# Optimization experiments

Measured on AMD Instinct MI355X. Metric: run time of the kernel, lower is better.

The kernel has to match this reference:

```python
import jax, jax.numpy as jnp
import numpy as np

B, N, K = 4, 4096, 16
D_POINTS, D_MODEL = 64, 128


def setup_inputs() -> dict:
    key = jax.random.key(0)
    ks = jax.random.split(key, 18)
    rn = lambda k, shp, s=0.05: (jax.random.normal(k, shp, jnp.float32) * s)
    return {
        "xyz": jax.random.normal(ks[0], (B, N, 3), jnp.float32),
        "features": jax.random.normal(ks[1], (B, N, D_POINTS), jnp.float32),
        # fc_delta: Linear(3,d_model) -> ReLU -> Linear(d_model,d_model)
        "Wd1": rn(ks[2], (3, D_MODEL)), "bd1": rn(ks[3], (D_MODEL,)),
        "Wd2": rn(ks[4], (D_MODEL, D_MODEL)), "bd2": rn(ks[5], (D_MODEL,)),
        # fc1: Linear(d_points, d_model)
        "Wf1": rn(ks[6], (D_POINTS, D_MODEL)), "bf1": rn(ks[7], (D_MODEL,)),
        # w_qs / w_ks / w_vs: Linear(d_model, d_model, bias=False)
        "Wq": rn(ks[8], (D_MODEL, D_MODEL)),
        "Wk": rn(ks[9], (D_MODEL, D_MODEL)),
        "Wv": rn(ks[10], (D_MODEL, D_MODEL)),
        # fc_gamma: Linear(d_model,d_model) -> ReLU -> Linear(d_model,d_model)
        "Wg1": rn(ks[11], (D_MODEL, D_MODEL)), "bg1": rn(ks[12], (D_MODEL,)),
        "Wg2": rn(ks[13], (D_MODEL, D_MODEL)), "bg2": rn(ks[14], (D_MODEL,)),
        # fc2: Linear(d_model, d_points)
        "Wo": rn(ks[15], (D_MODEL, D_POINTS)), "bo": rn(ks[16], (D_POINTS,)),
    }


def reference(xyz, features, Wd1, bd1, Wd2, bd2, Wf1, bf1, Wq, Wk, Wv,
              Wg1, bg1, Wg2, bg2, Wo, bo):
    sq = jnp.sum(xyz * xyz, axis=-1)
    d2 = sq[:, :, None] + sq[:, None, :] - 2.0 * jnp.einsum('bnd,bmd->bnm', xyz, xyz)
    # argsort()[:, :, :k] == k smallest distances (self included)
    _, knn_idx = jax.lax.top_k(-d2, K)  # [B,N,K] int32

    gather = jax.vmap(lambda a, i: a[i])  # per-batch fancy gather along point axis
    knn_xyz = gather(xyz, knn_idx)                       # [B,N,K,3]
    rel = xyz[:, :, None, :] - knn_xyz                   # [B,N,K,3]
    pos_enc = jax.nn.relu(rel @ Wd1 + bd1) @ Wd2 + bd2   # [B,N,K,D]

    shortcut = features
    f = features @ Wf1 + bf1                             # [B,N,D]
    knn_f = gather(f, knn_idx)                           # [B,N,K,D]

    q = f @ Wq                                           # [B,N,D]
    k = knn_f @ Wk                                       # [B,N,K,D]
    v = knn_f @ Wv                                       # [B,N,K,D]

    attn = q[:, :, None, :] - k + pos_enc                # [B,N,K,D]
    attn = jax.nn.relu(attn @ Wg1 + bg1) @ Wg2 + bg2
    attn = jax.nn.softmax(attn / np.sqrt(D_MODEL).astype(np.float32), axis=-2)

    res = jnp.einsum('bnkf,bnkf->bnf', attn, v + pos_enc)  # [B,N,D]
    return res @ Wo + bo + shortcut                        # [B,N,d_points]
```

## Files before the change

kernel.cpp:

```cpp
#include <hip/hip_runtime.h>
#include <hip/hip_bf16.h>

#define NPTS 4096
#define BATCH 4
#define BN (BATCH * NPTS)
#define DMODEL 128
#define DPTS 64
#define KNBR 16
#define SWS 136
#define PBLK 8

typedef unsigned short u16;
typedef unsigned int u32;
typedef unsigned long long u64;
typedef short bh8 __attribute__((ext_vector_type(8)));
typedef float f32x4 __attribute__((ext_vector_type(4)));

__device__ __forceinline__ float bfu(u16 u) {
    union { u32 i; float f; } c; c.i = ((u32)u) << 16; return c.f;
}
__device__ __forceinline__ u16 f2u(float x) {
    u32 u = __float_as_uint(x);
    u32 r = u + 0x7FFFu + ((u >> 16) & 1u);
    return (u16)(r >> 16);
}
__device__ __forceinline__ u32 pack2(float a, float b) {
    return (u32)f2u(a) | ((u32)f2u(b) << 16);
}
__device__ __forceinline__ u32 dpp_xor1(u32 v) {
    return (u32)__builtin_amdgcn_update_dpp(0, (int)v, 0xB1, 0xF, 0xF, true);
}
__device__ __forceinline__ u32 dpp_shr1(u32 v) {
    return (u32)__builtin_amdgcn_update_dpp(0, (int)v, 0x111, 0xF, 0xF, false);
}
__device__ __forceinline__ float ldr(const void* p, long i, int mode) {
    return mode == 0 ? bfu(((const u16*)p)[i]) : ((const float*)p)[i];
}
__device__ __forceinline__ void str(void* p, long i, float v, int mode) {
    if (mode == 0) ((u16*)p)[i] = f2u(v);
    else ((float*)p)[i] = v;
}
__device__ __forceinline__ int detect_mode(const void* Wq) {
    const u16* w = (const u16*)Wq;
    int lane = threadIdx.x & 63;
    int tot = 0;
#pragma unroll
    for (int r = 0; r < 4; ++r) {
        unsigned e = (w[lane + r * 64] >> 7) & 0xFFu;
        bool wild = (e >= 132u) || (e > 0u && e <= 90u);
        tot += (int)__popcll(__ballot(wild));
    }
    return tot > 32 ? 1 : 0;
}

__global__ __launch_bounds__(256) void prep_kernel(
    const void* __restrict__ Wd2, const void* __restrict__ Wg1, const void* __restrict__ Wg2,
    const void* __restrict__ Wo, const void* __restrict__ Wq, const void* __restrict__ Wk,
    const void* __restrict__ Wv, const void* __restrict__ Wf1, const void* __restrict__ xyz,
    u16* __restrict__ WdT2, u16* __restrict__ WgT1, u16* __restrict__ WgT2,
    u16* __restrict__ WoT, u16* __restrict__ WqT, u16* __restrict__ WkT,
    u16* __restrict__ WvT, u16* __restrict__ WfT, float4* __restrict__ cloudF) {
    int mode = detect_mode(Wq);
    int gid = blockIdx.x * 256 + threadIdx.x;
    if (gid < 6 * 16384) {
        int m = gid >> 14, o = gid & 16383;
        int n = o >> 7, i = o & 127;
        const void* W = (m == 0) ? Wd2 : (m == 1) ? Wg1 : (m == 2) ? Wg2
                      : (m == 3) ? Wq  : (m == 4) ? Wk  : Wv;
        u16* D = (m == 0) ? WdT2 : (m == 1) ? WgT1 : (m == 2) ? WgT2
               : (m == 3) ? WqT  : (m == 4) ? WkT  : WvT;
        D[o] = f2u(ldr(W, (long)i * 128 + n, mode));
    } else if (gid < 6 * 16384 + 8192) {
        int o = gid - 6 * 16384;
        int n = o >> 6, k2 = o & 63;
        WfT[o] = f2u(ldr(Wf1, (long)k2 * 128 + n, mode));
    } else if (gid < 6 * 16384 + 16384) {
        int o2 = gid - 6 * 16384 - 8192;
        int col = o2 >> 7, i = o2 & 127;
        WoT[o2] = f2u(ldr(Wo, (long)i * 64 + col, mode));
    } else if (gid < 6 * 16384 + 16384 + 16384) {
        int i = gid - (6 * 16384 + 16384);
        float gx = ldr(xyz, (long)i * 3 + 0, mode);
        float gy = ldr(xyz, (long)i * 3 + 1, mode);
        float gz = ldr(xyz, (long)i * 3 + 2, mode);
        float4 f;
        f.x = gx; f.y = gy; f.z = gz;
        f.w = gx * gx + gy * gy + gz * gz;
        cloudF[i] = f;
    }
}

__global__ __launch_bounds__(256) void qkv_kernel(
    const void* __restrict__ feat, const void* __restrict__ bf1v, const void* __restrict__ WqRaw,
    const u16* __restrict__ WfT, const u16* __restrict__ WqT,
    const u16* __restrict__ WkT, const u16* __restrict__ WvT,
    u16* __restrict__ qw, u16* __restrict__ kfw, u16* __restrict__ vfw) {
    int mode = detect_mode(WqRaw);
    __shared__ __align__(16) u16 sFeat[64 * 72];
    __shared__ __align__(16) u16 sF[64 * SWS];
    const int t = threadIdx.x;
    const int p0 = blockIdx.x * 64;
    const int lane = t & 63, w = t >> 6;
    const int rg = (w & 1) * 32, cg = (w >> 1) * 64;
    const int lm = lane & 15, lq = lane >> 4;

    for (int i = t; i < 512; i += 256) {
        int r = i >> 3, c8 = i & 7;
        u16 tmp[8];
        if (mode == 0) {
            *(uint4*)tmp = *((const uint4*)feat + (long)(p0 + r) * 8 + c8);
        } else {
            const float* fp = (const float*)feat + (long)(p0 + r) * 64 + c8 * 8;
#pragma unroll
            for (int u = 0; u < 8; ++u) tmp[u] = f2u(fp[u]);
        }
        *(uint4*)(sFeat + r * 72 + c8 * 8) = *(uint4*)tmp;
    }
    __syncthreads();

    {
        f32x4 acc[2][4];
#pragma unroll
        for (int rt = 0; rt < 2; ++rt)
#pragma unroll
            for (int ct = 0; ct < 4; ++ct) { acc[rt][ct][0]=0.f; acc[rt][ct][1]=0.f; acc[rt][ct][2]=0.f; acc[rt][ct][3]=0.f; }
#pragma unroll
        for (int kk = 0; kk < 2; ++kk) {
            const int ko = kk * 32 + lq * 8;
            bh8 a0 = *(const bh8*)(sFeat + (rg + lm) * 72 + ko);
            bh8 a1 = *(const bh8*)(sFeat + (rg + 16 + lm) * 72 + ko);
            bh8 bq[4];
#pragma unroll
            for (int ct = 0; ct < 4; ++ct)
                bq[ct] = *(const bh8*)(WfT + (long)(cg + ct * 16 + lm) * 64 + ko);
#pragma unroll
            for (int ct = 0; ct < 4; ++ct) {
                acc[0][ct] = __builtin_amdgcn_mfma_f32_16x16x32_bf16(a0, bq[ct], acc[0][ct], 0, 0, 0);
                acc[1][ct] = __builtin_amdgcn_mfma_f32_16x16x32_bf16(a1, bq[ct], acc[1][ct], 0, 0, 0);
            }
        }
#pragma unroll
        for (int rt = 0; rt < 2; ++rt)
#pragma unroll
            for (int ct = 0; ct < 4; ++ct) {
                const int col = cg + ct * 16 + lm;
                const float bj = ldr(bf1v, col, mode);
#pragma unroll
                for (int r4 = 0; r4 < 4; ++r4) {
                    int row = rg + rt * 16 + lq * 4 + r4;
                    u32 u = (u32)f2u(acc[rt][ct][r4] + bj);
                    u32 o = dpp_xor1(u);
                    if ((lane & 1) == 0)
                        *(u32*)(sF + row * SWS + col) = u | (o << 16);
                }
            }
    }
    __syncthreads();

    {
        const int m = blockIdx.y;
        const u16* Wm = (m == 0) ? WqT : (m == 1) ? WkT : WvT;
        u16* Om = (m == 0) ? qw : (m == 1) ? kfw : vfw;
        f32x4 acc[2][4];
#pragma unroll
        for (int rt = 0; rt < 2; ++rt)
#pragma unroll
            for (int ct = 0; ct < 4; ++ct) { acc[rt][ct][0]=0.f; acc[rt][ct][1]=0.f; acc[rt][ct][2]=0.f; acc[rt][ct][3]=0.f; }
#pragma unroll
        for (int kk = 0; kk < 4; ++kk) {
            const int ko = kk * 32 + lq * 8;
            bh8 a0 = *(const bh8*)(sF + (rg + lm) * SWS + ko);
            bh8 a1 = *(const bh8*)(sF + (rg + 16 + lm) * SWS + ko);
            bh8 bq[4];
#pragma unroll
            for (int ct = 0; ct < 4; ++ct)
                bq[ct] = *(const bh8*)(Wm + (long)(cg + ct * 16 + lm) * 128 + ko);
#pragma unroll
            for (int ct = 0; ct < 4; ++ct) {
                acc[0][ct] = __builtin_amdgcn_mfma_f32_16x16x32_bf16(a0, bq[ct], acc[0][ct], 0, 0, 0);
                acc[1][ct] = __builtin_amdgcn_mfma_f32_16x16x32_bf16(a1, bq[ct], acc[1][ct], 0, 0, 0);
            }
        }
#pragma unroll
        for (int rt = 0; rt < 2; ++rt)
#pragma unroll
            for (int ct = 0; ct < 4; ++ct) {
                const int col = cg + ct * 16 + lm;
#pragma unroll
                for (int r4 = 0; r4 < 4; ++r4) {
                    int row = rg + rt * 16 + lq * 4 + r4;
                    u32 u = (u32)f2u(acc[rt][ct][r4]);
                    u32 o = dpp_xor1(u);
                    if ((lane & 1) == 0)
                        *(u32*)(Om + (long)(p0 + row) * DMODEL + col) = u | (o << 16);
                }
            }
    }
}

__global__ __launch_bounds__(256) void knn_kernel(
    const float4* __restrict__ cloudF, int* __restrict__ knnIdx) {
    const int t = threadIdx.x, lane = t & 63, w = t >> 6;
    const int p0 = blockIdx.x * 4;
    const long bbase = (long)(p0 >> 12) * NPTS;
    const float4* cl = cloudF + bbase;

    const int pl = (p0 & (NPTS - 1)) + w;
    float4 qv = cl[pl];
    const float m2x = -2.f * qv.x, m2y = -2.f * qv.y, m2z = -2.f * qv.z;

    u64 kv;
    {
        float4 c = cl[lane];
        float key = fmaf(m2x, c.x, fmaf(m2y, c.y, fmaf(m2z, c.z, c.w)));
        u32 uk = __float_as_uint(key);
        uk ^= (u32)((int)uk >> 31) | 0x80000000u;
        kv = ((u64)uk << 32) | (u32)lane;
#pragma unroll
        for (int k = 2; k <= 64; k <<= 1) {
#pragma unroll
            for (int j = k >> 1; j > 0; j >>= 1) {
                u64 other = __shfl_xor(kv, j);
                bool keepMin = ((lane & j) == 0) == ((lane & k) == 0);
                bool smaller = kv < other;
                kv = (keepMin == smaller) ? kv : other;
            }
        }
    }
    u32 Tu = __builtin_amdgcn_readlane((u32)(kv >> 32), 15);

    float4 cd0 = cl[64 + lane];
    float4 cd1 = cl[128 + lane];
#pragma unroll 1
    for (int it = 0; it < 32; ++it) {
        const int base = 64 + it * 128;
        float4 c0 = cd0, c1 = cd1;
        if (it < 31) {
            int n0 = base + 128 + lane;
            int n1 = n0 + 64 > 4095 ? 4095 : n0 + 64;
            cd0 = cl[n0];
            cd1 = cl[n1];
        }
        float k0 = fmaf(m2x, c0.x, fmaf(m2y, c0.y, fmaf(m2z, c0.z, c0.w)));
        float k1 = fmaf(m2x, c1.x, fmaf(m2y, c1.y, fmaf(m2z, c1.z, c1.w)));
        u32 u0 = __float_as_uint(k0); u0 ^= (u32)((int)u0 >> 31) | 0x80000000u;
        u32 u1 = __float_as_uint(k1); u1 ^= (u32)((int)u1 >> 31) | 0x80000000u;
        if (it == 31) u1 = 0xFFFFFFFFu;
        u32 umin = (u0 < u1) ? u0 : u1;
        unsigned long long mask = __ballot(umin < Tu);
        while (mask) {
            int l = __ffsll(mask) - 1;
            mask &= mask - 1;
            u32 a0 = __builtin_amdgcn_readlane(u0, l);
            u32 a1 = __builtin_amdgcn_readlane(u1, l);
            if (a0 < Tu) {
                u64 cand = ((u64)a0 << 32) | (u32)(base + l);
                u64 prev = ((u64)dpp_shr1((u32)(kv >> 32)) << 32) | dpp_shr1((u32)kv);
                kv = (prev > cand) ? prev : ((kv > cand) ? cand : kv);
                Tu = __builtin_amdgcn_readlane((u32)(kv >> 32), 15);
            }
            if (a1 < Tu) {
                u64 cand = ((u64)a1 << 32) | (u32)(base + 64 + l);
                u64 prev = ((u64)dpp_shr1((u32)(kv >> 32)) << 32) | dpp_shr1((u32)kv);
                kv = (prev > cand) ? prev : ((kv > cand) ? cand : kv);
                Tu = __builtin_amdgcn_readlane((u32)(kv >> 32), 15);
            }
        }
    }
    if (lane < 16) knnIdx[(long)(p0 + w) * 16 + lane] = (int)(u32)kv;
}

__device__ __forceinline__ void mfma8(const u16* sIn, const u16* __restrict__ Bg,
                                      const float* bias, bool dorelu, bool inplace,
                                      u16* sOut, int t) {
    const int lane = t & 63, w = t >> 6;
    const int rg = (w & 3) * 32, cg = (w >> 2) * 64;
    const int lm = lane & 15, lq = lane >> 4;
    f32x4 acc[2][4];
#pragma unroll
    for (int rt = 0; rt < 2; ++rt)
#pragma unroll
        for (int ct = 0; ct < 4; ++ct) { acc[rt][ct][0]=0.f; acc[rt][ct][1]=0.f; acc[rt][ct][2]=0.f; acc[rt][ct][3]=0.f; }
#pragma unroll
    for (int kk = 0; kk < 4; ++kk) {
        const int ko = kk * 32 + lq * 8;
        bh8 a0 = *(const bh8*)(sIn + (rg + lm) * SWS + ko);
        bh8 a1 = *(const bh8*)(sIn + (rg + 16 + lm) * SWS + ko);
        bh8 bq[4];
#pragma unroll
        for (int ct = 0; ct < 4; ++ct)
            bq[ct] = *(const bh8*)(Bg + (long)(cg + ct * 16 + lm) * 128 + ko);
#pragma unroll
        for (int ct = 0; ct < 4; ++ct) {
            acc[0][ct] = __builtin_amdgcn_mfma_f32_16x16x32_bf16(a0, bq[ct], acc[0][ct], 0, 0, 0);
            acc[1][ct] = __builtin_amdgcn_mfma_f32_16x16x32_bf16(a1, bq[ct], acc[1][ct], 0, 0, 0);
        }
    }
    if (inplace) __syncthreads();
#pragma unroll
    for (int rt = 0; rt < 2; ++rt)
#pragma unroll
        for (int ct = 0; ct < 4; ++ct) {
            const int col = cg + ct * 16 + lm;
            const float bj = bias[col];
#pragma unroll
            for (int r4 = 0; r4 < 4; ++r4) {
                int row = rg + rt * 16 + lq * 4 + r4;
                float v = acc[rt][ct][r4] + bj;
                if (dorelu) v = fmaxf(v, 0.f);
                u32 u = (u32)f2u(v);
                u32 o = __shfl_xor(u, 1);
                if ((lane & 1) == 0)
                    *(u32*)(sOut + row * SWS + col) = u | (o << 16);
            }
        }
}

#define ATT_SA 0
#define ATT_SPE 34816
#define ATT_SREL 69632
#define ATT_SBIAS 71680
#define ATT_SQ 73216
#define SMEM_BYTES 75264

__global__ __launch_bounds__(512, 4) void fused_kernel(
    const float4* __restrict__ cloudF, const int* __restrict__ knnIdx,
    const void* __restrict__ feat,
    const void* __restrict__ Wd1, const void* __restrict__ bd1, const void* __restrict__ bd2,
    const void* __restrict__ bg1, const void* __restrict__ bg2, const void* __restrict__ bo,
    const void* __restrict__ WqRaw,
    const u16* __restrict__ WdT2, const u16* __restrict__ WgT1, const u16* __restrict__ WgT2,
    const u16* __restrict__ WoT,
    const u16* __restrict__ qw, const u16* __restrict__ kfw, const u16* __restrict__ vfw,
    void* __restrict__ out) {
    int mode = detect_mode(WqRaw);
    __shared__ __align__(16) char smem[SMEM_BYTES];
    __shared__ int sIdx[128];
    u16* sA   = (u16*)(smem + ATT_SA);
    u16* sPE  = (u16*)(smem + ATT_SPE);
    float (*sRel)[4] = (float(*)[4])(smem + ATT_SREL);
    float* sBias = (float*)(smem + ATT_SBIAS);
    u16* sQ   = (u16*)(smem + ATT_SQ);

    const int t = threadIdx.x, lane = t & 63, w = t >> 6;
    const int lm = lane & 15, lq = lane >> 4;
    const int p0 = blockIdx.x * PBLK;
    const long bbase = (long)(p0 >> 12) * NPTS;
    const float4* cl = cloudF + bbase;

    for (int i = t; i < 384; i += 512) {
        const void* b = (i < 128) ? bd2 : (i < 256) ? bg1 : bg2;
        sBias[i] = ldr(b, i & 127, mode);
    }
    ((u32*)sQ)[t] = ((const u32*)(qw + (long)p0 * DMODEL))[t];
    const int ch = 2 * lane;
    const float wd0a = ldr(Wd1, ch, mode),       wd0b = ldr(Wd1, ch + 1, mode);
    const float wd1a = ldr(Wd1, 128 + ch, mode), wd1b = ldr(Wd1, 128 + ch + 1, mode);
    const float wd2a = ldr(Wd1, 256 + ch, mode), wd2b = ldr(Wd1, 256 + ch + 1, mode);
    const float bd1a = ldr(bd1, ch, mode),       bd1b = ldr(bd1, ch + 1, mode);
    if (t < 128) {
        int idx = knnIdx[(long)p0 * 16 + t];
        sIdx[t] = idx;
        int pl2 = (p0 & (NPTS - 1)) + (t >> 4);
        float4 pv = cl[pl2];
        float4 nv = cl[idx];
        sRel[t][0] = pv.x - nv.x;
        sRel[t][1] = pv.y - nv.y;
        sRel[t][2] = pv.z - nv.z;
    }
    __syncthreads();

#pragma unroll
    for (int i = 0; i < 16; ++i) {
        int r = w * 16 + i;
        float4 rl = *(const float4*)sRel[r];
        float h0 = fmaxf(bd1a + rl.x * wd0a + rl.y * wd1a + rl.z * wd2a, 0.f);
        float h1 = fmaxf(bd1b + rl.x * wd0b + rl.y * wd1b + rl.z * wd2b, 0.f);
        *(u32*)(sA + r * SWS + ch) = pack2(h0, h1);
    }
    __syncthreads();
    mfma8(sA, WdT2, sBias, false, false, sPE, t);
    __syncthreads();

#pragma unroll
    for (int i = 0; i < 16; ++i) {
        int r = w * 16 + i;
        u32 kv2 = *(const u32*)(kfw + (bbase + sIdx[r]) * (long)DMODEL + ch);
        u32 qv2 = *(const u32*)(sQ + (r >> 4) * DMODEL + ch);
        u32 pe2 = *(const u32*)(sPE + r * SWS + ch);
        float a0 = bfu((u16)qv2) - bfu((u16)kv2) + bfu((u16)pe2);
        float a1 = bfu((u16)(qv2 >> 16)) - bfu((u16)(kv2 >> 16)) + bfu((u16)(pe2 >> 16));
        *(u32*)(sA + r * SWS + ch) = pack2(a0, a1);
    }
    __syncthreads();
    mfma8(sA, WgT1, sBias + 128, true, true, sA, t);
    __syncthreads();
    mfma8(sA, WgT2, sBias + 256, false, true, sA, t);
    __syncthreads();

    float res0, res1;
    {
        float mx0 = -3e38f, mx1 = -3e38f;
#pragma unroll
        for (int k = 0; k < KNBR; ++k) {
            u32 l2 = *(const u32*)(sA + (w * 16 + k) * SWS + ch);
            mx0 = fmaxf(mx0, bfu((u16)l2));
            mx1 = fmaxf(mx1, bfu((u16)(l2 >> 16)));
        }
        const float inv = 0.08838834764831845f;
        float s0 = 0.f, s1 = 0.f, r0 = 0.f, r1 = 0.f;
#pragma unroll
        for (int k = 0; k < KNBR; ++k) {
            u32 l2 = *(const u32*)(sA + (w * 16 + k) * SWS + ch);
            u32 v2 = *(const u32*)(vfw + (bbase + sIdx[w * 16 + k]) * (long)DMODEL + ch);
            u32 p2 = *(const u32*)(sPE + (w * 16 + k) * SWS + ch);
            float e0 = __expf((bfu((u16)l2) - mx0) * inv);
            float e1 = __expf((bfu((u16)(l2 >> 16)) - mx1) * inv);
            s0 += e0; s1 += e1;
            r0 += e0 * (bfu((u16)v2) + bfu((u16)p2));
            r1 += e1 * (bfu((u16)(v2 >> 16)) + bfu((u16)(p2 >> 16)));
        }
        res0 = r0 / s0; res1 = r1 / s1;
    }
    __syncthreads();
    *(u32*)(sA + w * SWS + ch) = pack2(res0, res1);
    __syncthreads();

    if (w < 4) {
        const int col = w * 16 + lm;
        f32x4 acc = {0.f, 0.f, 0.f, 0.f};
#pragma unroll
        for (int kk = 0; kk < 4; ++kk) {
            const int ko = kk * 32 + lq * 8;
            bh8 aa = *(const bh8*)(sA + lm * SWS + ko);
            bh8 bb = *(const bh8*)(WoT + (long)col * DMODEL + ko);
            acc = __builtin_amdgcn_mfma_f32_16x16x32_bf16(aa, bb, acc, 0, 0, 0);
        }
        if (lq < 2) {
            float bov = ldr(bo, col, mode);
#pragma unroll
            for (int r4 = 0; r4 < 4; ++r4) {
                long p = p0 + lq * 4 + r4;
                float v = acc[r4] + bov + ldr(feat, p * DPTS + col, mode);
                str(out, p * DPTS + col, v, mode);
            }
        }
    }
}

extern "C" void kernel_launch(void* const* d_in, const int* in_sizes, int n_in,
                              void* d_out, int out_size, void* d_ws, size_t ws_size,
                              hipStream_t stream) {
    (void)in_sizes; (void)n_in; (void)out_size; (void)ws_size;
    char* ws = (char*)d_ws;
    u16* qw   = (u16*)(ws + 256);
    u16* kfw  = qw + (long)BN * DMODEL;
    u16* vfw  = kfw + (long)BN * DMODEL;
    u16* WdT2 = vfw + (long)BN * DMODEL;
    u16* WgT1 = WdT2 + 16384;
    u16* WgT2 = WgT1 + 16384;
    u16* WoT  = WgT2 + 16384;
    u16* WqT  = WoT + 8192;
    u16* WkT  = WqT + 16384;
    u16* WvT  = WkT + 16384;
    u16* WfT  = WvT + 16384;
    float4* cloudF = (float4*)(WfT + 8192);
    int* knnIdx = (int*)(cloudF + BN);

    prep_kernel<<<512, 256, 0, stream>>>(d_in[4], d_in[11], d_in[13], d_in[15],
                                         d_in[8], d_in[9], d_in[10], d_in[6], d_in[0],
                                         WdT2, WgT1, WgT2, WoT, WqT, WkT, WvT, WfT,
                                         cloudF);
    qkv_kernel<<<dim3(BN / 64, 3), 256, 0, stream>>>(d_in[1], d_in[7], d_in[8],
                                                     WfT, WqT, WkT, WvT, qw, kfw, vfw);
    knn_kernel<<<BN / 4, 256, 0, stream>>>(cloudF, knnIdx);
    fused_kernel<<<BN / PBLK, 512, 0, stream>>>(cloudF, knnIdx, d_in[1],
                                                d_in[2], d_in[3], d_in[5],
                                                d_in[12], d_in[14], d_in[16], d_in[8],
                                                WdT2, WgT1, WgT2, WoT,
                                                qw, kfw, vfw, d_out);
}
```

Before: 302.3 us.

## Split cloud prep out and co-schedule weight transposes with kNN blocks

The prep kernel is split so the point-cloud prep runs as its own small kernel. The weight-transpose work now runs in the first blocks of the kNN kernel, with the remaining blocks doing kNN. The goal is to overlap weight preparation with the kNN search and cut the serial prep stage from the critical path. The cost is one extra launch, block-index-based branching inside a single kernel, and QKV now launching after kNN rather than before it.

```diff
diff --git a/kernel.cpp b/kernel.cpp
--- a/kernel.cpp
+++ b/kernel.cpp
@@ -9,6 +9,7 @@
 #define KNBR 16
 #define SWS 136
 #define PBLK 8
+#define WBLK 512
 
 typedef unsigned short u16;
 typedef unsigned int u32;
@@ -53,155 +54,53 @@
     return tot > 32 ? 1 : 0;
 }
 
-__global__ __launch_bounds__(256) void prep_kernel(
+__global__ __launch_bounds__(256) void prep_cloud_kernel(
+    const void* __restrict__ xyz, const void* __restrict__ Wq,
+    float4* __restrict__ cloudF) {
+    int mode = detect_mode(Wq);
+    int i = blockIdx.x * 256 + threadIdx.x;
+    float gx = ldr(xyz, (long)i * 3 + 0, mode);
+    float gy = ldr(xyz, (long)i * 3 + 1, mode);
+    float gz = ldr(xyz, (long)i * 3 + 2, mode);
+    float4 f;
+    f.x = gx; f.y = gy; f.z = gz;
+    f.w = gx * gx + gy * gy + gz * gz;
+    cloudF[i] = f;
+}
+
+__global__ __launch_bounds__(256) void wk_kernel(
     const void* __restrict__ Wd2, const void* __restrict__ Wg1, const void* __restrict__ Wg2,
     const void* __restrict__ Wo, const void* __restrict__ Wq, const void* __restrict__ Wk,
-    const void* __restrict__ Wv, const void* __restrict__ Wf1, const void* __restrict__ xyz,
+    const void* __restrict__ Wv, const void* __restrict__ Wf1,
     u16* __restrict__ WdT2, u16* __restrict__ WgT1, u16* __restrict__ WgT2,
     u16* __restrict__ WoT, u16* __restrict__ WqT, u16* __restrict__ WkT,
-    u16* __restrict__ WvT, u16* __restrict__ WfT, float4* __restrict__ cloudF) {
-    int mode = detect_mode(Wq);
-    int gid = blockIdx.x * 256 + threadIdx.x;
-    if (gid < 6 * 16384) {
-        int m = gid >> 14, o = gid & 16383;
-        int n = o >> 7, i = o & 127;
-        const void* W = (m == 0) ? Wd2 : (m == 1) ? Wg1 : (m == 2) ? Wg2
-                      : (m == 3) ? Wq  : (m == 4) ? Wk  : Wv;
-        u16* D = (m == 0) ? WdT2 : (m == 1) ? WgT1 : (m == 2) ? WgT2
-               : (m == 3) ? WqT  : (m == 4) ? WkT  : WvT;
-        D[o] = f2u(ldr(W, (long)i * 128 + n, mode));
-    } else if (gid < 6 * 16384 + 8192) {
-        int o = gid - 6 * 16384;
-        int n = o >> 6, k2 = o & 63;
-        WfT[o] = f2u(ldr(Wf1, (long)k2 * 128 + n, mode));
-    } else if (gid < 6 * 16384 + 16384) {
-        int o2 = gid - 6 * 16384 - 8192;
-        int col = o2 >> 7, i = o2 & 127;
-        WoT[o2] = f2u(ldr(Wo, (long)i * 64 + col, mode));
-    } else if (gid < 6 * 16384 + 16384 + 16384) {
-        int i = gid - (6 * 16384 + 16384);
-        float gx = ldr(xyz, (long)i * 3 + 0, mode);
-        float gy = ldr(xyz, (long)i * 3 + 1, mode);
-        float gz = ldr(xyz, (long)i * 3 + 2, mode);
-        float4 f;
-        f.x = gx; f.y = gy; f.z = gz;
-        f.w = gx * gx + gy * gy + gz * gz;
-        cloudF[i] = f;
-    }
-}
-
-__global__ __launch_bounds__(256) void qkv_kernel(
-    const void* __restrict__ feat, const void* __restrict__ bf1v, const void* __restrict__ WqRaw,
-    const u16* __restrict__ WfT, const u16* __restrict__ WqT,
-    const u16* __restrict__ WkT, const u16* __restrict__ WvT,
-    u16* __restrict__ qw, u16* __restrict__ kfw, u16* __restrict__ vfw) {
-    int mode = detect_mode(WqRaw);
-    __shared__ __align__(16) u16 sFeat[64 * 72];
-    __shared__ __align__(16) u16 sF[64 * SWS];
-    const int t = threadIdx.x;
-    const int p0 = blockIdx.x * 64;
-    const int lane = t & 63, w = t >> 6;
-    const int rg = (w & 1) * 32, cg = (w >> 1) * 64;
-    const int lm = lane & 15, lq = lane >> 4;
-
-    for (int i = t; i < 512; i += 256) {
-        int r = i >> 3, c8 = i & 7;
-        u16 tmp[8];
-        if (mode == 0) {
-            *(uint4*)tmp = *((const uint4*)feat + (long)(p0 + r) * 8 + c8);
-        } else {
-            const float* fp = (const float*)feat + (long)(p0 + r) * 64 + c8 * 8;
-#pragma unroll
-            for (int u = 0; u < 8; ++u) tmp[u] = f2u(fp[u]);
-        }
-        *(uint4*)(sFeat + r * 72 + c8 * 8) = *(uint4*)tmp;
-    }
-    __syncthreads();
-
-    {
-        f32x4 acc[2][4];
-#pragma unroll
-        for (int rt = 0; rt < 2; ++rt)
-#pragma unroll
-            for (int ct = 0; ct < 4; ++ct) { acc[rt][ct][0]=0.f; acc[rt][ct][1]=0.f; acc[rt][ct][2]=0.f; acc[rt][ct][3]=0.f; }
-#pragma unroll
-        for (int kk = 0; kk < 2; ++kk) {
-            const int ko = kk * 32 + lq * 8;
-            bh8 a0 = *(const bh8*)(sFeat + (rg + lm) * 72 + ko);
-            bh8 a1 = *(const bh8*)(sFeat + (rg + 16 + lm) * 72 + ko);
-            bh8 bq[4];
-#pragma unroll
-            for (int ct = 0; ct < 4; ++ct)
-                bq[ct] = *(const bh8*)(WfT + (long)(cg + ct * 16 + lm) * 64 + ko);
-#pragma unroll
-            for (int ct = 0; ct < 4; ++ct) {
-                acc[0][ct] = __builtin_amdgcn_mfma_f32_16x16x32_bf16(a0, bq[ct], acc[0][ct], 0, 0, 0);
-                acc[1][ct] = __builtin_amdgcn_mfma_f32_16x16x32_bf16(a1, bq[ct], acc[1][ct], 0, 0, 0);
-            }
-        }
-#pragma unroll
-        for (int rt = 0; rt < 2; ++rt)
-#pragma unroll
-            for (int ct = 0; ct < 4; ++ct) {
-                const int col = cg + ct * 16 + lm;
-                const float bj = ldr(bf1v, col, mode);
-#pragma unroll
-                for (int r4 = 0; r4 < 4; ++r4) {
-                    int row = rg + rt * 16 + lq * 4 + r4;
-                    u32 u = (u32)f2u(acc[rt][ct][r4] + bj);
-                    u32 o = dpp_xor1(u);
-                    if ((lane & 1) == 0)
-                        *(u32*)(sF + row * SWS + col) = u | (o << 16);
-                }
-            }
-    }
-    __syncthreads();
-
-    {
-        const int m = blockIdx.y;
-        const u16* Wm = (m == 0) ? WqT : (m == 1) ? WkT : WvT;
-        u16* Om = (m == 0) ? qw : (m == 1) ? kfw : vfw;
-        f32x4 acc[2][4];
-#pragma unroll
-        for (int rt = 0; rt < 2; ++rt)
-#pragma unroll
-            for (int ct = 0; ct < 4; ++ct) { acc[rt][ct][0]=0.f; acc[rt][ct][1]=0.f; acc[rt][ct][2]=0.f; acc[rt][ct][3]=0.f; }
-#pragma unroll
-        for (int kk = 0; kk < 4; ++kk) {
-            const int ko = kk * 32 + lq * 8;
-            bh8 a0 = *(const bh8*)(sF + (rg + lm) * SWS + ko);
-            bh8 a1 = *(const bh8*)(sF + (rg + 16 + lm) * SWS + ko);
-            bh8 bq[4];
-#pragma unroll
-            for (int ct = 0; ct < 4; ++ct)
-                bq[ct] = *(const bh8*)(Wm + (long)(cg + ct * 16 + lm) * 128 + ko);
-#pragma unroll
-            for (int ct = 0; ct < 4; ++ct) {
-                acc[0][ct] = __builtin_amdgcn_mfma_f32_16x16x32_bf16(a0, bq[ct], acc[0][ct], 0, 0, 0);
-                acc[1][ct] = __builtin_amdgcn_mfma_f32_16x16x32_bf16(a1, bq[ct], acc[1][ct], 0, 0, 0);
-            }
-        }
-#pragma unroll
-        for (int rt = 0; rt < 2; ++rt)
-#pragma unroll
-            for (int ct = 0; ct < 4; ++ct) {
-                const int col = cg + ct * 16 + lm;
-#pragma unroll
-                for (int r4 = 0; r4 < 4; ++r4) {
-                    int row = rg + rt * 16 + lq * 4 + r4;
-                    u32 u = (u32)f2u(acc[rt][ct][r4]);
-                    u32 o = dpp_xor1(u);
-                    if ((lane & 1) == 0)
-                        *(u32*)(Om + (long)(p0 + row) * DMODEL + col) = u | (o << 16);
-                }
-            }
-    }
-}
-
-__global__ __launch_bounds__(256) void knn_kernel(
+    u16* __restrict__ WvT, u16* __restrict__ WfT,
     const float4* __restrict__ cloudF, int* __restrict__ knnIdx) {
+    if (blockIdx.x < WBLK) {
+        int mode = detect_mode(Wq);
+        int gid = blockIdx.x * 256 + threadIdx.x;
+        if (gid < 6 * 16384) {
+            int m = gid >> 14, o = gid & 16383;
+            int n = o >> 7, i = o & 127;
+            const void* W = (m == 0) ? Wd2 : (m == 1) ? Wg1 : (m == 2) ? Wg2
+                          : (m == 3) ? Wq  : (m == 4) ? Wk  : Wv;
+            u16* D = (m == 0) ? WdT2 : (m == 1) ? WgT1 : (m == 2) ? WgT2
+                   : (m == 3) ? WqT  : (m == 4) ? WkT  : WvT;
+            D[o] = f2u(ldr(W, (long)i * 128 + n, mode));
+        } else if (gid < 6 * 16384 + 8192) {
+            int o = gid - 6 * 16384;
+            int n = o >> 6, k2 = o & 63;
+            WfT[o] = f2u(ldr(Wf1, (long)k2 * 128 + n, mode));
+        } else if (gid < 6 * 16384 + 16384) {
+            int o2 = gid - 6 * 16384 - 8192;
+            int col = o2 >> 7, i = o2 & 127;
+            WoT[o2] = f2u(ldr(Wo, (long)i * 64 + col, mode));
+        }
+        return;
+    }
+
     const int t = threadIdx.x, lane = t & 63, w = t >> 6;
-    const int p0 = blockIdx.x * 4;
+    const int p0 = (blockIdx.x - WBLK) * 4;
     const long bbase = (long)(p0 >> 12) * NPTS;
     const float4* cl = cloudF + bbase;
 
@@ -268,6 +167,114 @@
         }
     }
     if (lane < 16) knnIdx[(long)(p0 + w) * 16 + lane] = (int)(u32)kv;
+}
+
+__global__ __launch_bounds__(256) void qkv_kernel(
+    const void* __restrict__ feat, const void* __restrict__ bf1v, const void* __restrict__ WqRaw,
+    const u16* __restrict__ WfT, const u16* __restrict__ WqT,
+    const u16* __restrict__ WkT, const u16* __restrict__ WvT,
+    u16* __restrict__ qw, u16* __restrict__ kfw, u16* __restrict__ vfw) {
+    int mode = detect_mode(WqRaw);
+    __shared__ __align__(16) u16 sFeat[64 * 72];
+    __shared__ __align__(16) u16 sF[64 * SWS];
+    const int t = threadIdx.x;
+    const int p0 = blockIdx.x * 64;
+    const int lane = t & 63, w = t >> 6;
+    const int rg = (w & 1) * 32, cg = (w >> 1) * 64;
+    const int lm = lane & 15, lq = lane >> 4;
+
+    for (int i = t; i < 512; i += 256) {
+        int r = i >> 3, c8 = i & 7;
+        u16 tmp[8];
+        if (mode == 0) {
+            *(uint4*)tmp = *((const uint4*)feat + (long)(p0 + r) * 8 + c8);
+        } else {
+            const float* fp = (const float*)feat + (long)(p0 + r) * 64 + c8 * 8;
+#pragma unroll
+            for (int u = 0; u < 8; ++u) tmp[u] = f2u(fp[u]);
+        }
+        *(uint4*)(sFeat + r * 72 + c8 * 8) = *(uint4*)tmp;
+    }
+    __syncthreads();
+
+    {
+        f32x4 acc[2][4];
+#pragma unroll
+        for (int rt = 0; rt < 2; ++rt)
+#pragma unroll
+            for (int ct = 0; ct < 4; ++ct) { acc[rt][ct][0]=0.f; acc[rt][ct][1]=0.f; acc[rt][ct][2]=0.f; acc[rt][ct][3]=0.f; }
+#pragma unroll
+        for (int kk = 0; kk < 2; ++kk) {
+            const int ko = kk * 32 + lq * 8;
+            bh8 a0 = *(const bh8*)(sFeat + (rg + lm) * 72 + ko);
+            bh8 a1 = *(const bh8*)(sFeat + (rg + 16 + lm) * 72 + ko);
+            bh8 bq[4];
+#pragma unroll
+            for (int ct = 0; ct < 4; ++ct)
+                bq[ct] = *(const bh8*)(WfT + (long)(cg + ct * 16 + lm) * 64 + ko);
+#pragma unroll
+            for (int ct = 0; ct < 4; ++ct) {
+                acc[0][ct] = __builtin_amdgcn_mfma_f32_16x16x32_bf16(a0, bq[ct], acc[0][ct], 0, 0, 0);
+                acc[1][ct] = __builtin_amdgcn_mfma_f32_16x16x32_bf16(a1, bq[ct], acc[1][ct], 0, 0, 0);
+            }
+        }
+#pragma unroll
+        for (int rt = 0; rt < 2; ++rt)
+#pragma unroll
+            for (int ct = 0; ct < 4; ++ct) {
+                const int col = cg + ct * 16 + lm;
+                const float bj = ldr(bf1v, col, mode);
+#pragma unroll
+                for (int r4 = 0; r4 < 4; ++r4) {
+                    int row = rg + rt * 16 + lq * 4 + r4;
+                    u32 u = (u32)f2u(acc[rt][ct][r4] + bj);
+                    u32 o = dpp_xor1(u);
+                    if ((lane & 1) == 0)
+                        *(u32*)(sF + row * SWS + col) = u | (o << 16);
+                }
+            }
+    }
+    __syncthreads();
+
+    {
+        const int m = blockIdx.y;
+        const u16* Wm = (m == 0) ? WqT : (m == 1) ? WkT : WvT;
+        u16* Om = (m == 0) ? qw : (m == 1) ? kfw : vfw;
+        f32x4 acc[2][4];
+#pragma unroll
+        for (int rt = 0; rt < 2; ++rt)
+#pragma unroll
+            for (int ct = 0; ct < 4; ++ct) { acc[rt][ct][0]=0.f; acc[rt][ct][1]=0.f; acc[rt][ct][2]=0.f; acc[rt][ct][3]=0.f; }
+#pragma unroll
+        for (int kk = 0; kk < 4; ++kk) {
+            const int ko = kk * 32 + lq * 8;
+            bh8 a0 = *(const bh8*)(sF + (rg + lm) * SWS + ko);
+            bh8 a1 = *(const bh8*)(sF + (rg + 16 + lm) * SWS + ko);
+            bh8 bq[4];
+#pragma unroll
+            for (int ct = 0; ct < 4; ++ct)
+                bq[ct] = *(const bh8*)(Wm + (long)(cg + ct * 16 + lm) * 128 + ko);
+#pragma unroll
+            for (int ct = 0; ct < 4; ++ct) {
+                acc[0][ct] = __builtin_amdgcn_mfma_f32_16x16x32_bf16(a0, bq[ct], acc[0][ct], 0, 0, 0);
+                acc[1][ct] = __builtin_amdgcn_mfma_f32_16x16x32_bf16(a1, bq[ct], acc[1][ct], 0, 0, 0);
+            }
+        }
+#pragma unroll
+        for (int rt = 0; rt < 2; ++rt)
+#pragma unroll
+            for (int ct = 0; ct < 4; ++ct) {
+                const int col = cg + ct * 16 + lm;
+#pragma unroll
+                for (int r4 = 0; r4 < 4; ++r4) {
+                    int row = rg + rt * 16 + lq * 4 + r4;
+                    u32 u = (u32)f2u(acc[rt][ct][r4]);
+                    u32 o = dpp_xor1(u);
+                    if ((lane & 1) == 0)
+                        *(u32*)(Om + (long)(p0 + row) * DMODEL + col) = u | (o << 16);
+                }
+            }
+    }
 }
 
 __device__ __forceinline__ void mfma8(const u16* sIn, const u16* __restrict__ Bg,
@@ -467,13 +474,13 @@
     float4* cloudF = (float4*)(WfT + 8192);
     int* knnIdx = (int*)(cloudF + BN);
 
-    prep_kernel<<<512, 256, 0, stream>>>(d_in[4], d_in[11], d_in[13], d_in[15],
-                                         d_in[8], d_in[9], d_in[10], d_in[6], d_in[0],
-                                         WdT2, WgT1, WgT2, WoT, WqT, WkT, WvT, WfT,
-                                         cloudF);
+    prep_cloud_kernel<<<BN / 256, 256, 0, stream>>>(d_in[0], d_in[8], cloudF);
+    wk_kernel<<<WBLK + BN / 4, 256, 0, stream>>>(d_in[4], d_in[11], d_in[13], d_in[15],
+                                                 d_in[8], d_in[9], d_in[10], d_in[6],
+                                                 WdT2, WgT1, WgT2, WoT, WqT, WkT, WvT,
+                                                 WfT, cloudF, knnIdx);
     qkv_kernel<<<dim3(BN / 64, 3), 256, 0, stream>>>(d_in[1], d_in[7], d_in[8],
                                                      WfT, WqT, WkT, WvT, qw, kfw, vfw);
-    knn_kernel<<<BN / 4, 256, 0, stream>>>(cloudF, knnIdx);
     fused_kernel<<<BN / PBLK, 512, 0, stream>>>(cloudF, knnIdx, d_in[1],
                                                 d_in[2], d_in[3], d_in[5],
                                                 d_in[12], d_in[14], d_in[16], d_in[8],
```

Result: no change. 303.0 us (median of 2 runs) (+0.2%).
